# Kernel tuning notes

Measured on AMD Instinct MI355X. Metric: run time of the kernel, lower is better.

## Reference

```python
import jax, jax.numpy as jnp
import numpy as np

ALPHA = 0.2          # LeakyReLU slope
NEG_BIG = -9e15      # mask value from the torch code
LN_EPS = 1e-5        # torch LayerNorm default eps
GAT_SCALE = 1.0


def _layer_norm(x, g, b):
    mu = x.mean(-1, keepdims=True)
    var = ((x - mu) ** 2).mean(-1, keepdims=True)
    return (x - mu) * jax.lax.rsqrt(var + LN_EPS) * g + b


def _gat_layer(h, adj, W, a, concat):
    # h: [B,N,Fin], adj: [N,N] weighted, W: [Fin,Fout], a: [2*Fout,1]
    Wh = jnp.einsum('bnf,fo->bno', h, W)                 # [B,N,Fout]
    Fo = W.shape[1]
    a_i, a_j = a[:Fo, 0], a[Fo:, 0]
    # e[b,i,j] = leakyrelu(Wh[b,i].a_i + Wh[b,j].a_j)  (== cat([Wh_i,Wh_j]) @ a)
    e = jax.nn.leaky_relu(
        (Wh @ a_i)[:, :, None] + (Wh @ a_j)[:, None, :], ALPHA)  # [B,N,N]
    att = jnp.where(adj[None, :, :] > 0, e, NEG_BIG)
    att = jax.nn.softmax(att, axis=2)
    att = att * adj[None, :, :]
    att = att / (att.sum(axis=2, keepdims=True) + 1e-8)
    h_prime = jnp.einsum('bij,bjo->bio', att, Wh)        # [B,N,Fout]
    return jax.nn.elu(h_prime) if concat else h_prime


def setup_inputs() -> dict:
    B, N, H, ID = 1024, 128, 64, 8
    GIN = 1 + ID  # node_feat_dim = 0
    key = jax.random.key(0)
    ks = jax.random.split(key, 20)
    # sparse weighted adjacency with self-loops
    w = jax.random.uniform(ks[0], (N, N))
    m = (jax.random.uniform(ks[1], (N, N)) < 0.3).astype(jnp.float32)
    adj = w * m + jnp.eye(N, dtype=jnp.float32)
    sc = lambda k, s: jax.random.normal(k, s, jnp.float32) * 0.1
    return {
        'c_values': jax.random.normal(ks[2], (B, N), jnp.float32),
        'adj': adj,
        'agent_emb': sc(ks[3], (N, ID)),
        'W1': sc(ks[4], (GIN, H)), 'a1': sc(ks[5], (2 * H, 1)),
        'W2': sc(ks[6], (H, H)),   'a2': sc(ks[7], (2 * H, 1)),
        'ln1_g': jnp.ones((H,)), 'ln1_b': jnp.zeros((H,)),
        'ln2_g': jnp.ones((H,)), 'ln2_b': jnp.zeros((H,)),
        'head_gat_w': sc(ks[8], (H, 1)), 'head_gat_b': jnp.zeros((1,)),
        'mlp1_w': sc(ks[9], (N, H)),  'mlp1_b': jnp.zeros((H,)),
        'mlp2_w': sc(ks[10], (H, H)), 'mlp2_b': jnp.zeros((H,)),
        'head_mlp_w': sc(ks[11], (H, 1)), 'head_mlp_b': jnp.zeros((1,)),
        'gate1_w': sc(ks[12], (N, H)), 'gate1_b': jnp.zeros((H,)),
        'gate2_w': sc(ks[13], (H, 1)), 'gate2_b': jnp.full((1,), -5.0),
    }


def reference(c_values, adj, agent_emb, W1, a1, W2, a2,
              ln1_g, ln1_b, ln2_g, ln2_b, head_gat_w, head_gat_b,
              mlp1_w, mlp1_b, mlp2_w, mlp2_b, head_mlp_w, head_mlp_b,
              gate1_w, gate1_b, gate2_w, gate2_b):
    B, N = c_values.shape
    # node features: [c_value, agent_id_embedding]
    id_feat = jnp.broadcast_to(agent_emb[None], (B, N, agent_emb.shape[1]))
    x_g = jnp.concatenate([c_values[..., None], id_feat], axis=-1)  # [B,N,9]
    h1 = _gat_layer(x_g, adj, W1, a1, concat=True)
    h1 = _layer_norm(h1, ln1_g, ln1_b)
    h2 = _gat_layer(h1, adj, W2, a2, concat=False)
    h = jax.nn.relu(h2 + h1)
    h = _layer_norm(h, ln2_g, ln2_b)
    q_gat = h.mean(axis=1) @ head_gat_w + head_gat_b                # [B,1]
    x_m = jax.nn.relu(c_values @ mlp1_w + mlp1_b)
    x_m = jax.nn.relu(x_m @ mlp2_w + mlp2_b)
    q_mlp = x_m @ head_mlp_w + head_mlp_b                           # [B,1]
    gate = jax.nn.sigmoid(
        jax.nn.relu(c_values @ gate1_w + gate1_b) @ gate2_w + gate2_b)
    return q_mlp + gate * GAT_SCALE * q_gat
```

## Files before the change

kernel.cpp:

```cpp
#include <hip/hip_runtime.h>

typedef unsigned short u16;
typedef unsigned int u32;
typedef short v8s __attribute__((ext_vector_type(8)));
typedef float v4f __attribute__((ext_vector_type(4)));
typedef float v2f __attribute__((ext_vector_type(2)));

__device__ __forceinline__ float bflo(u32 d){union{u32 i;float f;}u;u.i=d<<16;return u.f;}
__device__ __forceinline__ float bfhi(u32 d){union{u32 i;float f;}u;u.i=d&0xffff0000u;return u.f;}
__device__ __forceinline__ u16 f2bfr(float f){union{float f;u32 i;}u;u.f=f;return (u16)((u.i+0x8000u)>>16);}
__device__ __forceinline__ u32 pk2bf(float a,float b){
    union{float f;u32 i;}ua,ub; ua.f=a; ub.f=b;
    u32 x = ua.i + 0x8000u, y = ub.i + 0x8000u;
    return __builtin_amdgcn_perm(y, x, 0x07060302);
}
__device__ __forceinline__ v8s pack8(const float* w){
    union { uint4 u; v8s v; } c;
    c.u.x = pk2bf(w[0],w[1]); c.u.y = pk2bf(w[2],w[3]);
    c.u.z = pk2bf(w[4],w[5]); c.u.w = pk2bf(w[6],w[7]);
    return c.v;
}

__device__ __forceinline__ void flash_att(
    int wv, int l15, int q4,
    const float* __restrict__ ADJ,
    const float* __restrict__ sEi, const float* __restrict__ sFi,
    const float* __restrict__ sEj, const float* __restrict__ sFj,
    const u16* __restrict__ sWhT,
    v4f acc[2][4], float invD[2])
{
    const int r0 = 16*wv + l15, r1 = r0 + 64;
    const v2f Ei0 = {sEi[r0], sEi[r0]}, Fi0 = {sFi[r0], sFi[r0]};
    const v2f Ei1 = {sEi[r1], sEi[r1]}, Fi1 = {sFi[r1], sFi[r1]};
    v2f D0 = {0.f,0.f}, D1 = {0.f,0.f};
    #pragma unroll
    for (int s = 0; s < 2; ++s)
        #pragma unroll
        for (int ct = 0; ct < 4; ++ct) acc[s][ct] = (v4f){0.f,0.f,0.f,0.f};

    #pragma unroll
    for (int ks = 0; ks < 4; ++ks) {
        const int ko = ks*32 + q4*8;
        const v2f* Ejp = (const v2f*)(sEj + ko);
        const v2f* Fjp = (const v2f*)(sFj + ko);
        const v2f* A0p = (const v2f*)(ADJ + r0*128 + ko);
        const v2f* A1p = (const v2f*)(ADJ + r1*128 + ko);
        union { u32 u[4]; v8s v; } P0, P1;
        #pragma unroll
        for (int p = 0; p < 4; ++p) {
            v2f E = Ejp[p], F = Fjp[p];
            v2f a0 = A0p[p], a1 = A1p[p];
            v2f m0 = __builtin_elementwise_max(Ei0*E, Fi0*F);
            v2f m1 = __builtin_elementwise_max(Ei1*E, Fi1*F);
            v2f x0 = m0 * a0;
            v2f x1 = m1 * a1;
            D0 += x0; D1 += x1;
            P0.u[p] = pk2bf(x0.x, x0.y);
            P1.u[p] = pk2bf(x1.x, x1.y);
        }
        #pragma unroll
        for (int ct = 0; ct < 4; ++ct) {
            v8s B = *(const v8s*)(sWhT + (16*ct + l15)*136 + ko);
            acc[0][ct] = __builtin_amdgcn_mfma_f32_16x16x32_bf16(P0.v, B, acc[0][ct], 0,0,0);
            acc[1][ct] = __builtin_amdgcn_mfma_f32_16x16x32_bf16(P1.v, B, acc[1][ct], 0,0,0);
        }
    }
    float d0 = D0.x + D0.y, d1 = D1.x + D1.y;
    d0 += __shfl_xor(d0, 16); d0 += __shfl_xor(d0, 32);
    d1 += __shfl_xor(d1, 16); d1 += __shfl_xor(d1, 32);
    invD[0] = 1.f / d0; invD[1] = 1.f / d1;
}

__global__ __launch_bounds__(256, 5) void graphmixer_kernel(
    const float* __restrict__ C,
    const float* __restrict__ ADJ,
    const float* __restrict__ EMB,
    const float* __restrict__ W1,
    const float* __restrict__ A1,
    const float* __restrict__ W2,
    const float* __restrict__ A2,
    const float* __restrict__ LN1G, const float* __restrict__ LN1B,
    const float* __restrict__ LN2G, const float* __restrict__ LN2B,
    const float* __restrict__ HGW,  const float* __restrict__ HGB,
    const float* __restrict__ MLP1W, const float* __restrict__ MLP1B,
    const float* __restrict__ MLP2W, const float* __restrict__ MLP2B,
    const float* __restrict__ HMW,  const float* __restrict__ HMB,
    const float* __restrict__ G1W,  const float* __restrict__ G1B,
    const float* __restrict__ G2W,  const float* __restrict__ G2B,
    float* __restrict__ OUT)
{
    const int b = blockIdx.x, t = threadIdx.x;
    const int lane = t & 63, wv = t >> 6;
    const int l15 = lane & 15, q4 = lane >> 4;

    __shared__ __align__(16) unsigned char smem[26272];
    u16*   R1   = (u16*)(smem);
    float* sEi  = (float*)(smem + 18432);
    float* sFi  = (float*)(smem + 18944);
    float* sEj  = (float*)(smem + 19456);
    float* sFj  = (float*)(smem + 19968);
    float* sScr = (float*)(smem + 20480);
    float* v2i  = (float*)(smem + 21024);
    float* v2j  = (float*)(smem + 21280);
    float* v1i  = (float*)(smem + 21536);
    float* v1j  = (float*)(smem + 21600);
    float* sEmb = (float*)(smem + 21664);
    float* sC   = (float*)(smem + 25760);
    float* colp = (float*)(smem + 21664);

    const float* Cb = C + b*128;

    if (wv == 0) {
        #pragma unroll
        for (int q = 0; q < 4; ++q)
            ((float4*)sEmb)[lane + 64*q] = ((const float4*)EMB)[lane + 64*q];
        if (lane < 32) ((float4*)sC)[lane] = ((const float4*)Cb)[lane];
        if (lane >= 32 && lane < 41) {
            int f = lane - 32; float a = 0.f;
            for (int q = 0; q < 16; ++q) {
                float4 w = *(const float4*)(W1 + f*64 + q*4);
                float4 x = *(const float4*)(A1 + q*4);
                a += w.x*x.x + w.y*x.y + w.z*x.z + w.w*x.w;
            }
            v1i[f] = a;
        } else if (lane >= 48 && lane < 57) {
            int f = lane - 48; float a = 0.f;
            for (int q = 0; q < 16; ++q) {
                float4 w = *(const float4*)(W1 + f*64 + q*4);
                float4 x = *(const float4*)(A1 + 64 + q*4);
                a += w.x*x.x + w.y*x.y + w.z*x.z + w.w*x.w;
            }
            v1j[f] = a;
        }
    } else if (wv == 3) {
        float ai = 0.f, aj = 0.f;
        for (int q = 0; q < 16; ++q) {
            float4 w  = *(const float4*)(W2 + lane*64 + q*4);
            float4 xi = *(const float4*)(A2 + q*4);
            float4 xj = *(const float4*)(A2 + 64 + q*4);
            ai += w.x*xi.x + w.y*xi.y + w.z*xi.z + w.w*xi.w;
            aj += w.x*xj.x + w.y*xj.y + w.z*xj.z + w.w*xj.w;
        }
        v2i[lane] = ai; v2j[lane] = aj;
    } else if (wv == 1) {
        float a = 0.f;
        for (int k = 0; k < 128; k += 4) {
            float4 c4 = *(const float4*)(Cb + k);
            a += c4.x*MLP1W[k*64+lane] + c4.y*MLP1W[(k+1)*64+lane]
               + c4.z*MLP1W[(k+2)*64+lane] + c4.w*MLP1W[(k+3)*64+lane];
        }
        sScr[lane] = fmaxf(a + MLP1B[lane], 0.f);
        float a2 = 0.f;
        for (int k = 0; k < 64; ++k) a2 += sScr[k] * MLP2W[k*64 + lane];
        float x2 = fmaxf(a2 + MLP2B[lane], 0.f);
        float p1 = x2 * HMW[lane];
        #pragma unroll
        for (int off = 32; off >= 1; off >>= 1) p1 += __shfl_down(p1, off);
        if (lane == 0) sScr[128] = p1 + HMB[0];
    } else {
        float a = 0.f;
        for (int k = 0; k < 128; k += 4) {
            float4 c4 = *(const float4*)(Cb + k);
            a += c4.x*G1W[k*64+lane] + c4.y*G1W[(k+1)*64+lane]
               + c4.z*G1W[(k+2)*64+lane] + c4.w*G1W[(k+3)*64+lane];
        }
        float g1 = fmaxf(a + G1B[lane], 0.f);
        float p2 = g1 * G2W[lane];
        #pragma unroll
        for (int off = 32; off >= 1; off >>= 1) p2 += __shfl_down(p2, off);
        if (lane == 0) sScr[129] = 1.f / (1.f + __expf(-(p2 + G2B[0])));
    }
    __syncthreads();

    {
        v8s Af[2];
        #pragma unroll
        for (int s = 0; s < 2; ++s) {
            const int row = 16*(wv + 4*s) + l15;
            float av[8];
            #pragma unroll
            for (int j = 0; j < 8; ++j) av[j] = 0.f;
            if (q4 == 0) {
                av[0] = sC[row];
                float4 e0 = *(const float4*)(sEmb + row*8);
                float4 e1 = *(const float4*)(sEmb + row*8 + 4);
                av[1]=e0.x; av[2]=e0.y; av[3]=e0.z; av[4]=e0.w;
                av[5]=e1.x; av[6]=e1.y; av[7]=e1.z;
            } else if (q4 == 1) {
                av[0] = sEmb[row*8 + 7];
            }
            Af[s] = pack8(av);
        }
        #pragma unroll
        for (int ct = 0; ct < 4; ++ct) {
            const int col = 16*ct + l15;
            float bv[8];
            #pragma unroll
            for (int j = 0; j < 8; ++j) bv[j] = 0.f;
            if (q4 == 0) {
                #pragma unroll
                for (int j = 0; j < 8; ++j) bv[j] = W1[j*64 + col];
            } else if (q4 == 1) {
                bv[0] = W1[8*64 + col];
            }
            v8s Bf1 = pack8(bv);
            v4f a0 = (v4f){0.f,0.f,0.f,0.f}, a1 = (v4f){0.f,0.f,0.f,0.f};
            a0 = __builtin_amdgcn_mfma_f32_16x16x32_bf16(Af[0], Bf1, a0, 0,0,0);
            a1 = __builtin_amdgcn_mfma_f32_16x16x32_bf16(Af[1], Bf1, a1, 0,0,0);
            uint2 p0, p1;
            p0.x = pk2bf(a0[0], a0[1]); p0.y = pk2bf(a0[2], a0[3]);
            p1.x = pk2bf(a1[0], a1[1]); p1.y = pk2bf(a1[2], a1[3]);
            *(uint2*)(R1 + col*136 + 16*wv      + 4*q4) = p0;
            *(uint2*)(R1 + col*136 + 16*(wv+4)  + 4*q4) = p1;
        }
    }
    {
        const int row = t >> 1;
        const float* vv = (t & 1) ? v1j : v1i;
        float c = sC[row];
        float4 e0 = *(const float4*)(sEmb + row*8);
        float4 e1 = *(const float4*)(sEmb + row*8 + 4);
        float e = c*vv[0] + e0.x*vv[1]+e0.y*vv[2]+e0.z*vv[3]+e0.w*vv[4]
                          + e1.x*vv[5]+e1.y*vv[6]+e1.z*vv[7]+e1.w*vv[8];
        if (t & 1) { sEj[row] = __expf(e); sFj[row] = __expf(0.2f*e); }
        else       { sEi[row] = __expf(e); sFi[row] = __expf(0.2f*e); }
    }
    __syncthreads();

    uint2 h1p[2][4];
    {
        v4f acc[2][4]; float invD[2];
        flash_att(wv, l15, q4, ADJ, sEi, sFi, sEj, sFj, R1, acc, invD);
        __syncthreads();

        float g4[4], b4[4], v2i4[4], v2j4[4];
        #pragma unroll
        for (int ct = 0; ct < 4; ++ct) {
            g4[ct] = LN1G[16*ct + l15]; b4[ct] = LN1B[16*ct + l15];
            v2i4[ct] = v2i[16*ct + l15]; v2j4[ct] = v2j[16*ct + l15];
        }
        #pragma unroll
        for (int s = 0; s < 2; ++s) {
            float hprev[4];
            #pragma unroll
            for (int reg = 0; reg < 4; ++reg) {
                const int ro = 16*(wv + 4*s) + 4*q4 + reg;
                const float rd = __shfl(invD[s], 4*q4 + reg);
                float x[4], s1 = 0.f, s2 = 0.f;
                #pragma unroll
                for (int ct = 0; ct < 4; ++ct) {
                    float v = acc[s][ct][reg] * rd;
                    v = (v > 0.f) ? v : (__expf(v) - 1.f);
                    x[ct] = v; s1 += v; s2 += v*v;
                }
                s1 += __shfl_xor(s1, 1); s2 += __shfl_xor(s2, 1);
                s1 += __shfl_xor(s1, 2); s2 += __shfl_xor(s2, 2);
                s1 += __shfl_xor(s1, 4); s2 += __shfl_xor(s2, 4);
                s1 += __shfl_xor(s1, 8); s2 += __shfl_xor(s2, 8);
                const float mean = s1 * (1.f/64.f);
                const float var  = s2 * (1.f/64.f) - mean*mean;
                const float rstd = rsqrtf(var + 1e-5f);
                float pi = 0.f, pj = 0.f;
                #pragma unroll
                for (int ct = 0; ct < 4; ++ct) {
                    float h = (x[ct] - mean) * rstd * g4[ct] + b4[ct];
                    R1[ro*72 + 16*ct + l15] = f2bfr(h);
                    pi += h * v2i4[ct]; pj += h * v2j4[ct];
                    if ((reg & 1) == 0) hprev[ct] = h;
                    else if (reg == 1)  h1p[s][ct].x = pk2bf(hprev[ct], h);
                    else                h1p[s][ct].y = pk2bf(hprev[ct], h);
                }
                pi += __shfl_xor(pi, 1); pj += __shfl_xor(pj, 1);
                pi += __shfl_xor(pi, 2); pj += __shfl_xor(pj, 2);
                pi += __shfl_xor(pi, 4); pj += __shfl_xor(pj, 4);
                pi += __shfl_xor(pi, 8); pj += __shfl_xor(pj, 8);
                if (l15 == 0) {
                    sEi[ro] = __expf(pi); sFi[ro] = __expf(0.2f*pi);
                    sEj[ro] = __expf(pj); sFj[ro] = __expf(0.2f*pj);
                }
            }
        }
    }
    __syncthreads();

    {
        v8s Afrag[2][2];
        #pragma unroll
        for (int s = 0; s < 2; ++s)
            #pragma unroll
            for (int ks = 0; ks < 2; ++ks)
                Afrag[s][ks] = *(const v8s*)(R1 + (16*(wv+4*s) + l15)*72 + ks*32 + q4*8);
        __syncthreads();

        v4f acc2[2][4];
        #pragma unroll
        for (int s = 0; s < 2; ++s)
            #pragma unroll
            for (int ct = 0; ct < 4; ++ct) acc2[s][ct] = (v4f){0.f,0.f,0.f,0.f};
        #pragma unroll
        for (int ks = 0; ks < 2; ++ks) {
            const int kb = ks*32 + q4*8;
            #pragma unroll
            for (int ct = 0; ct < 4; ++ct) {
                const float* wp = W2 + kb*64 + 16*ct + l15;
                float w8[8];
                #pragma unroll
                for (int j = 0; j < 8; ++j) w8[j] = wp[j*64];
                v8s Bf = pack8(w8);
                #pragma unroll
                for (int s = 0; s < 2; ++s)
                    acc2[s][ct] = __builtin_amdgcn_mfma_f32_16x16x32_bf16(Afrag[s][ks], Bf, acc2[s][ct], 0,0,0);
            }
        }
        #pragma unroll
        for (int s = 0; s < 2; ++s) {
            const int rb = 16*(wv+4*s) + 4*q4;
            #pragma unroll
            for (int ct = 0; ct < 4; ++ct) {
                const int col = 16*ct + l15;
                uint2 p;
                p.x = pk2bf(acc2[s][ct][0], acc2[s][ct][1]);
                p.y = pk2bf(acc2[s][ct][2], acc2[s][ct][3]);
                *(uint2*)(R1 + col*136 + rb) = p;
            }
        }
    }
    __syncthreads();

    {
        v4f acc[2][4]; float invD[2];
        flash_att(wv, l15, q4, ADJ, sEi, sFi, sEj, sFj, R1, acc, invD);

        float g4[4], b4[4], colsum[4];
        #pragma unroll
        for (int ct = 0; ct < 4; ++ct) {
            g4[ct] = LN2G[16*ct + l15]; b4[ct] = LN2B[16*ct + l15]; colsum[ct] = 0.f;
        }
        #pragma unroll
        for (int s = 0; s < 2; ++s) {
            #pragma unroll
            for (int reg = 0; reg < 4; ++reg) {
                const float rd = __shfl(invD[s], 4*q4 + reg);
                float x[4], s1 = 0.f, s2 = 0.f;
                #pragma unroll
                for (int ct = 0; ct < 4; ++ct) {
                    u32 w = (reg < 2) ? h1p[s][ct].x : h1p[s][ct].y;
                    float h1v = (reg & 1) ? bfhi(w) : bflo(w);
                    float v = fmaxf(acc[s][ct][reg] * rd + h1v, 0.f);
                    x[ct] = v; s1 += v; s2 += v*v;
                }
                s1 += __shfl_xor(s1, 1); s2 += __shfl_xor(s2, 1);
                s1 += __shfl_xor(s1, 2); s2 += __shfl_xor(s2, 2);
                s1 += __shfl_xor(s1, 4); s2 += __shfl_xor(s2, 4);
                s1 += __shfl_xor(s1, 8); s2 += __shfl_xor(s2, 8);
                const float mean = s1 * (1.f/64.f);
                const float var  = s2 * (1.f/64.f) - mean*mean;
                const float rstd = rsqrtf(var + 1e-5f);
                #pragma unroll
                for (int ct = 0; ct < 4; ++ct)
                    colsum[ct] += (x[ct] - mean) * rstd * g4[ct] + b4[ct];
            }
        }
        #pragma unroll
        for (int ct = 0; ct < 4; ++ct) {
            colsum[ct] += __shfl_xor(colsum[ct], 16);
            colsum[ct] += __shfl_xor(colsum[ct], 32);
        }
        if (lane < 16) {
            #pragma unroll
            for (int ct = 0; ct < 4; ++ct) colp[wv*64 + ct*16 + lane] = colsum[ct];
        }
    }
    __syncthreads();

    if (wv == 0) {
        float s = colp[lane] + colp[64 + lane] + colp[128 + lane] + colp[192 + lane];
        float p = s * (1.f/128.f) * HGW[lane];
        #pragma unroll
        for (int off = 32; off >= 1; off >>= 1) p += __shfl_down(p, off);
        if (lane == 0) OUT[b] = sScr[128] + sScr[129] * (p + HGB[0]);
    }
}

extern "C" void kernel_launch(void* const* d_in, const int* in_sizes, int n_in,
                              void* d_out, int out_size, void* d_ws, size_t ws_size,
                              hipStream_t stream) {
    (void)n_in; (void)out_size; (void)d_ws; (void)ws_size;
    const float* C     = (const float*)d_in[0];
    const float* ADJ   = (const float*)d_in[1];
    const float* EMB   = (const float*)d_in[2];
    const float* W1    = (const float*)d_in[3];
    const float* A1    = (const float*)d_in[4];
    const float* W2    = (const float*)d_in[5];
    const float* A2    = (const float*)d_in[6];
    const float* LN1G  = (const float*)d_in[7];
    const float* LN1B  = (const float*)d_in[8];
    const float* LN2G  = (const float*)d_in[9];
    const float* LN2B  = (const float*)d_in[10];
    const float* HGW   = (const float*)d_in[11];
    const float* HGB   = (const float*)d_in[12];
    const float* MLP1W = (const float*)d_in[13];
    const float* MLP1B = (const float*)d_in[14];
    const float* MLP2W = (const float*)d_in[15];
    const float* MLP2B = (const float*)d_in[16];
    const float* HMW   = (const float*)d_in[17];
    const float* HMB   = (const float*)d_in[18];
    const float* G1W   = (const float*)d_in[19];
    const float* G1B   = (const float*)d_in[20];
    const float* G2W   = (const float*)d_in[21];
    const float* G2B   = (const float*)d_in[22];

    const int B = in_sizes[0] / 128;

    graphmixer_kernel<<<dim3(B), dim3(256), 0, stream>>>(
        C, ADJ, EMB, W1, A1, W2, A2, LN1G, LN1B, LN2G, LN2B,
        HGW, HGB, MLP1W, MLP1B, MLP2W, MLP2B, HMW, HMB,
        G1W, G1B, G2W, G2B, (float*)d_out);
}
```

Baseline: 135.4 us.

## Process two batch elements per block to share adjacency loads and weights

Each block now handles two batch samples instead of one, so the grid is halved. Adjacency values read from global memory in the attention loop, the W2 B-fragments, and embedding/setup work are shared across both samples, and the extra independent MFMA chains give more instruction-level parallelism. In exchange, shared memory per block nearly doubles, register pressure rises (launch bounds drop from 5 to 2 blocks per CU), and only 512 blocks remain, which may underfill the GPU and reduce latency hiding.

Result: no change. 133.7 us (-1.2%).

```diff
diff --git a/kernel.cpp b/kernel.cpp
--- a/kernel.cpp
+++ b/kernel.cpp
@@ -21,57 +21,182 @@
     return c.v;
 }
 
-__device__ __forceinline__ void flash_att(
-    int wv, int l15, int q4,
-    const float* __restrict__ ADJ,
-    const float* __restrict__ sEi, const float* __restrict__ sFi,
-    const float* __restrict__ sEj, const float* __restrict__ sFj,
-    const u16* __restrict__ sWhT,
-    v4f acc[2][4], float invD[2])
+__device__ __forceinline__ void flash_att2(
+    int wv, int l15, int q4, const float* __restrict__ ADJ,
+    const float* __restrict__ sEiA, const float* __restrict__ sFiA,
+    const float* __restrict__ sEjA, const float* __restrict__ sFjA,
+    const float* __restrict__ sEiB, const float* __restrict__ sFiB,
+    const float* __restrict__ sEjB, const float* __restrict__ sFjB,
+    const u16* __restrict__ R1A, const u16* __restrict__ R1B,
+    v4f accA[2][4], v4f accB[2][4], float invDA[2], float invDB[2])
 {
     const int r0 = 16*wv + l15, r1 = r0 + 64;
-    const v2f Ei0 = {sEi[r0], sEi[r0]}, Fi0 = {sFi[r0], sFi[r0]};
-    const v2f Ei1 = {sEi[r1], sEi[r1]}, Fi1 = {sFi[r1], sFi[r1]};
-    v2f D0 = {0.f,0.f}, D1 = {0.f,0.f};
+    const v2f EiA0={sEiA[r0],sEiA[r0]}, FiA0={sFiA[r0],sFiA[r0]};
+    const v2f EiA1={sEiA[r1],sEiA[r1]}, FiA1={sFiA[r1],sFiA[r1]};
+    const v2f EiB0={sEiB[r0],sEiB[r0]}, FiB0={sFiB[r0],sFiB[r0]};
+    const v2f EiB1={sEiB[r1],sEiB[r1]}, FiB1={sFiB[r1],sFiB[r1]};
+    v2f DA0={0.f,0.f}, DA1={0.f,0.f}, DB0={0.f,0.f}, DB1={0.f,0.f};
     #pragma unroll
     for (int s = 0; s < 2; ++s)
         #pragma unroll
-        for (int ct = 0; ct < 4; ++ct) acc[s][ct] = (v4f){0.f,0.f,0.f,0.f};
+        for (int ct = 0; ct < 4; ++ct) {
+            accA[s][ct] = (v4f){0.f,0.f,0.f,0.f};
+            accB[s][ct] = (v4f){0.f,0.f,0.f,0.f};
+        }
 
     #pragma unroll
     for (int ks = 0; ks < 4; ++ks) {
         const int ko = ks*32 + q4*8;
-        const v2f* Ejp = (const v2f*)(sEj + ko);
-        const v2f* Fjp = (const v2f*)(sFj + ko);
+        const v2f* EjA = (const v2f*)(sEjA + ko);
+        const v2f* FjA = (const v2f*)(sFjA + ko);
+        const v2f* EjB = (const v2f*)(sEjB + ko);
+        const v2f* FjB = (const v2f*)(sFjB + ko);
         const v2f* A0p = (const v2f*)(ADJ + r0*128 + ko);
         const v2f* A1p = (const v2f*)(ADJ + r1*128 + ko);
-        union { u32 u[4]; v8s v; } P0, P1;
+        union { u32 u[4]; v8s v; } PA0, PA1, PB0, PB1;
         #pragma unroll
         for (int p = 0; p < 4; ++p) {
-            v2f E = Ejp[p], F = Fjp[p];
             v2f a0 = A0p[p], a1 = A1p[p];
-            v2f m0 = __builtin_elementwise_max(Ei0*E, Fi0*F);
-            v2f m1 = __builtin_elementwise_max(Ei1*E, Fi1*F);
-            v2f x0 = m0 * a0;
-            v2f x1 = m1 * a1;
-            D0 += x0; D1 += x1;
-            P0.u[p] = pk2bf(x0.x, x0.y);
-            P1.u[p] = pk2bf(x1.x, x1.y);
+            v2f EA = EjA[p], FA = FjA[p];
+            v2f EB = EjB[p], FB = FjB[p];
+            v2f xA0 = __builtin_elementwise_max(EiA0*EA, FiA0*FA) * a0;
+            v2f xA1 = __builtin_elementwise_max(EiA1*EA, FiA1*FA) * a1;
+            v2f xB0 = __builtin_elementwise_max(EiB0*EB, FiB0*FB) * a0;
+            v2f xB1 = __builtin_elementwise_max(EiB1*EB, FiB1*FB) * a1;
+            DA0 += xA0; DA1 += xA1; DB0 += xB0; DB1 += xB1;
+            PA0.u[p] = pk2bf(xA0.x, xA0.y);
+            PA1.u[p] = pk2bf(xA1.x, xA1.y);
+            PB0.u[p] = pk2bf(xB0.x, xB0.y);
+            PB1.u[p] = pk2bf(xB1.x, xB1.y);
         }
         #pragma unroll
         for (int ct = 0; ct < 4; ++ct) {
-            v8s B = *(const v8s*)(sWhT + (16*ct + l15)*136 + ko);
-            acc[0][ct] = __builtin_amdgcn_mfma_f32_16x16x32_bf16(P0.v, B, acc[0][ct], 0,0,0);
-            acc[1][ct] = __builtin_amdgcn_mfma_f32_16x16x32_bf16(P1.v, B, acc[1][ct], 0,0,0);
-        }
-    }
-    float d0 = D0.x + D0.y, d1 = D1.x + D1.y;
-    d0 += __shfl_xor(d0, 16); d0 += __shfl_xor(d0, 32);
-    d1 += __shfl_xor(d1, 16); d1 += __shfl_xor(d1, 32);
-    invD[0] = 1.f / d0; invD[1] = 1.f / d1;
-}
-
-__global__ __launch_bounds__(256, 5) void graphmixer_kernel(
+            v8s BA = *(const v8s*)(R1A + (16*ct + l15)*136 + ko);
+            v8s BB = *(const v8s*)(R1B + (16*ct + l15)*136 + ko);
+            accA[0][ct] = __builtin_amdgcn_mfma_f32_16x16x32_bf16(PA0.v, BA, accA[0][ct], 0,0,0);
+            accA[1][ct] = __builtin_amdgcn_mfma_f32_16x16x32_bf16(PA1.v, BA, accA[1][ct], 0,0,0);
+            accB[0][ct] = __builtin_amdgcn_mfma_f32_16x16x32_bf16(PB0.v, BB, accB[0][ct], 0,0,0);
+            accB[1][ct] = __builtin_amdgcn_mfma_f32_16x16x32_bf16(PB1.v, BB, accB[1][ct], 0,0,0);
+        }
+    }
+    float dA0 = DA0.x + DA0.y, dA1 = DA1.x + DA1.y;
+    float dB0 = DB0.x + DB0.y, dB1 = DB1.x + DB1.y;
+    dA0 += __shfl_xor(dA0, 16); dA0 += __shfl_xor(dA0, 32);
+    dA1 += __shfl_xor(dA1, 16); dA1 += __shfl_xor(dA1, 32);
+    dB0 += __shfl_xor(dB0, 16); dB0 += __shfl_xor(dB0, 32);
+    dB1 += __shfl_xor(dB1, 16); dB1 += __shfl_xor(dB1, 32);
+    invDA[0] = 1.f / dA0; invDA[1] = 1.f / dA1;
+    invDB[0] = 1.f / dB0; invDB[1] = 1.f / dB1;
+}
+
+__device__ __forceinline__ void epi1(
+    int wv, int l15, int q4,
+    const v4f acc[2][4], const float invD[2],
+    const float* __restrict__ LN1G, const float* __restrict__ LN1B,
+    const float* __restrict__ v2i, const float* __restrict__ v2j,
+    u16* __restrict__ R1,
+    float* __restrict__ sEi, float* __restrict__ sFi,
+    float* __restrict__ sEj, float* __restrict__ sFj,
+    uint2 h1p[2][4])
+{
+    float g4[4], b4[4], v2i4[4], v2j4[4];
+    #pragma unroll
+    for (int ct = 0; ct < 4; ++ct) {
+        g4[ct] = LN1G[16*ct + l15]; b4[ct] = LN1B[16*ct + l15];
+        v2i4[ct] = v2i[16*ct + l15]; v2j4[ct] = v2j[16*ct + l15];
+    }
+    #pragma unroll
+    for (int s = 0; s < 2; ++s) {
+        float hprev[4];
+        #pragma unroll
+        for (int reg = 0; reg < 4; ++reg) {
+            const int ro = 16*(wv + 4*s) + 4*q4 + reg;
+            const float rd = __shfl(invD[s], 4*q4 + reg);
+            float x[4], s1 = 0.f, s2 = 0.f;
+            #pragma unroll
+            for (int ct = 0; ct < 4; ++ct) {
+                float v = acc[s][ct][reg] * rd;
+                v = (v > 0.f) ? v : (__expf(v) - 1.f);
+                x[ct] = v; s1 += v; s2 += v*v;
+            }
+            s1 += __shfl_xor(s1, 1); s2 += __shfl_xor(s2, 1);
+            s1 += __shfl_xor(s1, 2); s2 += __shfl_xor(s2, 2);
+            s1 += __shfl_xor(s1, 4); s2 += __shfl_xor(s2, 4);
+            s1 += __shfl_xor(s1, 8); s2 += __shfl_xor(s2, 8);
+            const float mean = s1 * (1.f/64.f);
+            const float var  = s2 * (1.f/64.f) - mean*mean;
+            const float rstd = rsqrtf(var + 1e-5f);
+            float pi = 0.f, pj = 0.f;
+            #pragma unroll
+            for (int ct = 0; ct < 4; ++ct) {
+                float h = (x[ct] - mean) * rstd * g4[ct] + b4[ct];
+                R1[ro*72 + 16*ct + l15] = f2bfr(h);
+                pi += h * v2i4[ct]; pj += h * v2j4[ct];
+                if ((reg & 1) == 0) hprev[ct] = h;
+                else if (reg == 1)  h1p[s][ct].x = pk2bf(hprev[ct], h);
+                else                h1p[s][ct].y = pk2bf(hprev[ct], h);
+            }
+            pi += __shfl_xor(pi, 1); pj += __shfl_xor(pj, 1);
+            pi += __shfl_xor(pi, 2); pj += __shfl_xor(pj, 2);
+            pi += __shfl_xor(pi, 4); pj += __shfl_xor(pj, 4);
+            pi += __shfl_xor(pi, 8); pj += __shfl_xor(pj, 8);
+            if (l15 == 0) {
+                sEi[ro] = __expf(pi); sFi[ro] = __expf(0.2f*pi);
+                sEj[ro] = __expf(pj); sFj[ro] = __expf(0.2f*pj);
+            }
+        }
+    }
+}
+
+__device__ __forceinline__ void epi2(
+    int lane, int wv, int l15, int q4,
+    const v4f acc[2][4], const float invD[2],
+    const uint2 h1p[2][4],
+    const float* __restrict__ LN2G, const float* __restrict__ LN2B,
+    float* __restrict__ colp)
+{
+    float g4[4], b4[4], colsum[4];
+    #pragma unroll
+    for (int ct = 0; ct < 4; ++ct) {
+        g4[ct] = LN2G[16*ct + l15]; b4[ct] = LN2B[16*ct + l15]; colsum[ct] = 0.f;
+    }
+    #pragma unroll
+    for (int s = 0; s < 2; ++s) {
+        #pragma unroll
+        for (int reg = 0; reg < 4; ++reg) {
+            const float rd = __shfl(invD[s], 4*q4 + reg);
+            float x[4], s1 = 0.f, s2 = 0.f;
+            #pragma unroll
+            for (int ct = 0; ct < 4; ++ct) {
+                u32 w = (reg < 2) ? h1p[s][ct].x : h1p[s][ct].y;
+                float h1v = (reg & 1) ? bfhi(w) : bflo(w);
+                float v = fmaxf(acc[s][ct][reg] * rd + h1v, 0.f);
+                x[ct] = v; s1 += v; s2 += v*v;
+            }
+            s1 += __shfl_xor(s1, 1); s2 += __shfl_xor(s2, 1);
+            s1 += __shfl_xor(s1, 2); s2 += __shfl_xor(s2, 2);
+            s1 += __shfl_xor(s1, 4); s2 += __shfl_xor(s2, 4);
+            s1 += __shfl_xor(s1, 8); s2 += __shfl_xor(s2, 8);
+            const float mean = s1 * (1.f/64.f);
+            const float var  = s2 * (1.f/64.f) - mean*mean;
+            const float rstd = rsqrtf(var + 1e-5f);
+            #pragma unroll
+            for (int ct = 0; ct < 4; ++ct)
+                colsum[ct] += (x[ct] - mean) * rstd * g4[ct] + b4[ct];
+        }
+    }
+    #pragma unroll
+    for (int ct = 0; ct < 4; ++ct) {
+        colsum[ct] += __shfl_xor(colsum[ct], 16);
+        colsum[ct] += __shfl_xor(colsum[ct], 32);
+    }
+    if (lane < 16) {
+        #pragma unroll
+        for (int ct = 0; ct < 4; ++ct) colp[wv*64 + ct*16 + lane] = colsum[ct];
+    }
+}
+
+__global__ __launch_bounds__(256, 2) void graphmixer_kernel(
     const float* __restrict__ C,
     const float* __restrict__ ADJ,
     const float* __restrict__ EMB,
@@ -89,32 +214,43 @@
     const float* __restrict__ G2W,  const float* __restrict__ G2B,
     float* __restrict__ OUT)
 {
-    const int b = blockIdx.x, t = threadIdx.x;
+    const int bx = blockIdx.x, t = threadIdx.x;
     const int lane = t & 63, wv = t >> 6;
     const int l15 = lane & 15, q4 = lane >> 4;
-
-    __shared__ __align__(16) unsigned char smem[26272];
-    u16*   R1   = (u16*)(smem);
-    float* sEi  = (float*)(smem + 18432);
-    float* sFi  = (float*)(smem + 18944);
-    float* sEj  = (float*)(smem + 19456);
-    float* sFj  = (float*)(smem + 19968);
-    float* sScr = (float*)(smem + 20480);
-    float* v2i  = (float*)(smem + 21024);
-    float* v2j  = (float*)(smem + 21280);
-    float* v1i  = (float*)(smem + 21536);
-    float* v1j  = (float*)(smem + 21600);
-    float* sEmb = (float*)(smem + 21664);
-    float* sC   = (float*)(smem + 25760);
-    float* colp = (float*)(smem + 21664);
-
-    const float* Cb = C + b*128;
+    const int bA = 2*bx, bB = 2*bx + 1;
+
+    __shared__ __align__(16) unsigned char smem[47808];
+    u16*   R1A  = (u16*)(smem);
+    u16*   R1B  = (u16*)(smem + 18432);
+    float* sEiA = (float*)(smem + 36864);
+    float* sFiA = (float*)(smem + 37376);
+    float* sEjA = (float*)(smem + 37888);
+    float* sFjA = (float*)(smem + 38400);
+    float* sEiB = (float*)(smem + 38912);
+    float* sFiB = (float*)(smem + 39424);
+    float* sEjB = (float*)(smem + 39936);
+    float* sFjB = (float*)(smem + 40448);
+    float* v2i  = (float*)(smem + 40960);
+    float* v2j  = (float*)(smem + 41216);
+    float* v1i  = (float*)(smem + 41472);
+    float* v1j  = (float*)(smem + 41536);
+    float* sScrA= (float*)(smem + 41600);
+    float* sScrB= (float*)(smem + 42144);
+    float* sEmb = (float*)(smem + 42688);
+    float* sCA  = (float*)(smem + 46784);
+    float* sCB  = (float*)(smem + 47296);
+    float* colpA= (float*)(smem + 42688);
+    float* colpB= (float*)(smem + 43712);
+
+    const float* CbA = C + bA*128;
+    const float* CbB = C + bB*128;
 
     if (wv == 0) {
         #pragma unroll
         for (int q = 0; q < 4; ++q)
             ((float4*)sEmb)[lane + 64*q] = ((const float4*)EMB)[lane + 64*q];
-        if (lane < 32) ((float4*)sC)[lane] = ((const float4*)Cb)[lane];
+        if (lane < 32) ((float4*)sCA)[lane] = ((const float4*)CbA)[lane];
+        else           ((float4*)sCB)[lane - 32] = ((const float4*)CbB)[lane - 32];
         if (lane >= 32 && lane < 41) {
             int f = lane - 32; float a = 0.f;
             for (int q = 0; q < 16; ++q) {
@@ -132,7 +268,48 @@
             }
             v1j[f] = a;
         }
-    } else if (wv == 3) {
+        float a = 0.f;
+        for (int k = 0; k < 128; k += 4) {
+            float4 c4 = *(const float4*)(CbB + k);
+            a += c4.x*G1W[k*64+lane] + c4.y*G1W[(k+1)*64+lane]
+               + c4.z*G1W[(k+2)*64+lane] + c4.w*G1W[(k+3)*64+lane];
+        }
+        float g1 = fmaxf(a + G1B[lane], 0.f);
+        float p2 = g1 * G2W[lane];
+        #pragma unroll
+        for (int off = 32; off >= 1; off >>= 1) p2 += __shfl_down(p2, off);
+        if (lane == 0) sScrB[129] = 1.f / (1.f + __expf(-(p2 + G2B[0])));
+    } else if (wv == 1) {
+        float a = 0.f;
+        for (int k = 0; k < 128; k += 4) {
+            float4 c4 = *(const float4*)(CbA + k);
+            a += c4.x*MLP1W[k*64+lane] + c4.y*MLP1W[(k+1)*64+lane]
+               + c4.z*MLP1W[(k+2)*64+lane] + c4.w*MLP1W[(k+3)*64+lane];
+        }
+        sScrA[lane] = fmaxf(a + MLP1B[lane], 0.f);
+        float a2 = 0.f;
+        for (int k = 0; k < 64; ++k) a2 += sScrA[k] * MLP2W[k*64 + lane];
+        float x2 = fmaxf(a2 + MLP2B[lane], 0.f);
+        float p1 = x2 * HMW[lane];
+        #pragma unroll
+        for (int off = 32; off >= 1; off >>= 1) p1 += __shfl_down(p1, off);
+        if (lane == 0) sScrA[128] = p1 + HMB[0];
+    } else if (wv == 2) {
+        float a = 0.f;
+        for (int k = 0; k < 128; k += 4) {
+            float4 c4 = *(const float4*)(CbB + k);
+            a += c4.x*MLP1W[k*64+lane] + c4.y*MLP1W[(k+1)*64+lane]
+               + c4.z*MLP1W[(k+2)*64+lane] + c4.w*MLP1W[(k+3)*64+lane];
+        }
+        sScrB[lane] = fmaxf(a + MLP1B[lane], 0.f);
+        float a2 = 0.f;
+        for (int k = 0; k < 64; ++k) a2 += sScrB[k] * MLP2W[k*64 + lane];
+        float x2 = fmaxf(a2 + MLP2B[lane], 0.f);
+        float p1 = x2 * HMW[lane];
+        #pragma unroll
+        for (int off = 32; off >= 1; off >>= 1) p1 += __shfl_down(p1, off);
+        if (lane == 0) sScrB[128] = p1 + HMB[0];
+    } else {
         float ai = 0.f, aj = 0.f;
         for (int q = 0; q < 16; ++q) {
             float4 w  = *(const float4*)(W2 + lane*64 + q*4);
@@ -142,25 +319,9 @@
             aj += w.x*xj.x + w.y*xj.y + w.z*xj.z + w.w*xj.w;
         }
         v2i[lane] = ai; v2j[lane] = aj;
-    } else if (wv == 1) {
         float a = 0.f;
         for (int k = 0; k < 128; k += 4) {
-            float4 c4 = *(const float4*)(Cb + k);
-            a += c4.x*MLP1W[k*64+lane] + c4.y*MLP1W[(k+1)*64+lane]
-               + c4.z*MLP1W[(k+2)*64+lane] + c4.w*MLP1W[(k+3)*64+lane];
-        }
-        sScr[lane] = fmaxf(a + MLP1B[lane], 0.f);
-        float a2 = 0.f;
-        for (int k = 0; k < 64; ++k) a2 += sScr[k] * MLP2W[k*64 + lane];
-        float x2 = fmaxf(a2 + MLP2B[lane], 0.f);
-        float p1 = x2 * HMW[lane];
-        #pragma unroll
-        for (int off = 32; off >= 1; off >>= 1) p1 += __shfl_down(p1, off);
-        if (lane == 0) sScr[128] = p1 + HMB[0];
-    } else {
-        float a = 0.f;
-        for (int k = 0; k < 128; k += 4) {
-            float4 c4 = *(const float4*)(Cb + k);
+            float4 c4 = *(const float4*)(CbA + k);
             a += c4.x*G1W[k*64+lane] + c4.y*G1W[(k+1)*64+lane]
                + c4.z*G1W[(k+2)*64+lane] + c4.w*G1W[(k+3)*64+lane];
         }
@@ -168,28 +329,32 @@
         float p2 = g1 * G2W[lane];
         #pragma unroll
         for (int off = 32; off >= 1; off >>= 1) p2 += __shfl_down(p2, off);
-        if (lane == 0) sScr[129] = 1.f / (1.f + __expf(-(p2 + G2B[0])));
+        if (lane == 0) sScrA[129] = 1.f / (1.f + __expf(-(p2 + G2B[0])));
     }
     __syncthreads();
 
     {
-        v8s Af[2];
+        v8s AfA[2], AfB[2];
         #pragma unroll
         for (int s = 0; s < 2; ++s) {
             const int row = 16*(wv + 4*s) + l15;
-            float av[8];
-            #pragma unroll
-            for (int j = 0; j < 8; ++j) av[j] = 0.f;
+            float avA[8], avB[8];
+            #pragma unroll
+            for (int j = 0; j < 8; ++j) { avA[j] = 0.f; avB[j] = 0.f; }
             if (q4 == 0) {
-                av[0] = sC[row];
                 float4 e0 = *(const float4*)(sEmb + row*8);
                 float4 e1 = *(const float4*)(sEmb + row*8 + 4);
-                av[1]=e0.x; av[2]=e0.y; av[3]=e0.z; av[4]=e0.w;
-                av[5]=e1.x; av[6]=e1.y; av[7]=e1.z;
+                avA[0] = sCA[row];
+                avA[1]=e0.x; avA[2]=e0.y; avA[3]=e0.z; avA[4]=e0.w;
+                avA[5]=e1.x; avA[6]=e1.y; avA[7]=e1.z;
+                avB[0] = sCB[row];
+                avB[1]=e0.x; avB[2]=e0.y; avB[3]=e0.z; avB[4]=e0.w;
+                avB[5]=e1.x; avB[6]=e1.y; avB[7]=e1.z;
             } else if (q4 == 1) {
-                av[0] = sEmb[row*8 + 7];
-            }
-            Af[s] = pack8(av);
+                avA[0] = sEmb[row*8 + 7];
+                avB[0] = sEmb[row*8 + 7];
+            }
+            AfA[s] = pack8(avA); AfB[s] = pack8(avB);
         }
         #pragma unroll
         for (int ct = 0; ct < 4; ++ct) {
@@ -204,99 +369,76 @@
                 bv[0] = W1[8*64 + col];
             }
             v8s Bf1 = pack8(bv);
-            v4f a0 = (v4f){0.f,0.f,0.f,0.f}, a1 = (v4f){0.f,0.f,0.f,0.f};
-            a0 = __builtin_amdgcn_mfma_f32_16x16x32_bf16(Af[0], Bf1, a0, 0,0,0);
-            a1 = __builtin_amdgcn_mfma_f32_16x16x32_bf16(Af[1], Bf1, a1, 0,0,0);
-            uint2 p0, p1;
-            p0.x = pk2bf(a0[0], a0[1]); p0.y = pk2bf(a0[2], a0[3]);
-            p1.x = pk2bf(a1[0], a1[1]); p1.y = pk2bf(a1[2], a1[3]);
-            *(uint2*)(R1 + col*136 + 16*wv      + 4*q4) = p0;
-            *(uint2*)(R1 + col*136 + 16*(wv+4)  + 4*q4) = p1;
+            v4f aA0 = (v4f){0.f,0.f,0.f,0.f}, aA1 = (v4f){0.f,0.f,0.f,0.f};
+            v4f aB0 = (v4f){0.f,0.f,0.f,0.f}, aB1 = (v4f){0.f,0.f,0.f,0.f};
+            aA0 = __builtin_amdgcn_mfma_f32_16x16x32_bf16(AfA[0], Bf1, aA0, 0,0,0);
+            aA1 = __builtin_amdgcn_mfma_f32_16x16x32_bf16(AfA[1], Bf1, aA1, 0,0,0);
+            aB0 = __builtin_amdgcn_mfma_f32_16x16x32_bf16(AfB[0], Bf1, aB0, 0,0,0);
+            aB1 = __builtin_amdgcn_mfma_f32_16x16x32_bf16(AfB[1], Bf1, aB1, 0,0,0);
+            uint2 p;
+            p.x = pk2bf(aA0[0], aA0[1]); p.y = pk2bf(aA0[2], aA0[3]);
+            *(uint2*)(R1A + col*136 + 16*wv     + 4*q4) = p;
+            p.x = pk2bf(aA1[0], aA1[1]); p.y = pk2bf(aA1[2], aA1[3]);
+            *(uint2*)(R1A + col*136 + 16*(wv+4) + 4*q4) = p;
+            p.x = pk2bf(aB0[0], aB0[1]); p.y = pk2bf(aB0[2], aB0[3]);
+            *(uint2*)(R1B + col*136 + 16*wv     + 4*q4) = p;
+            p.x = pk2bf(aB1[0], aB1[1]); p.y = pk2bf(aB1[2], aB1[3]);
+            *(uint2*)(R1B + col*136 + 16*(wv+4) + 4*q4) = p;
         }
     }
     {
         const int row = t >> 1;
         const float* vv = (t & 1) ? v1j : v1i;
-        float c = sC[row];
         float4 e0 = *(const float4*)(sEmb + row*8);
         float4 e1 = *(const float4*)(sEmb + row*8 + 4);
-        float e = c*vv[0] + e0.x*vv[1]+e0.y*vv[2]+e0.z*vv[3]+e0.w*vv[4]
-                          + e1.x*vv[5]+e1.y*vv[6]+e1.z*vv[7]+e1.w*vv[8];
-        if (t & 1) { sEj[row] = __expf(e); sFj[row] = __expf(0.2f*e); }
-        else       { sEi[row] = __expf(e); sFi[row] = __expf(0.2f*e); }
+        float base = e0.x*vv[1]+e0.y*vv[2]+e0.z*vv[3]+e0.w*vv[4]
+                   + e1.x*vv[5]+e1.y*vv[6]+e1.z*vv[7]+e1.w*vv[8];
+        float eA = sCA[row]*vv[0] + base;
+        float eB = sCB[row]*vv[0] + base;
+        if (t & 1) {
+            sEjA[row] = __expf(eA); sFjA[row] = __expf(0.2f*eA);
+            sEjB[row] = __expf(eB); sFjB[row] = __expf(0.2f*eB);
+        } else {
+            sEiA[row] = __expf(eA); sFiA[row] = __expf(0.2f*eA);
+            sEiB[row] = __expf(eB); sFiB[row] = __expf(0.2f*eB);
+        }
     }
     __syncthreads();
 
-    uint2 h1p[2][4];
+    uint2 h1pA[2][4], h1pB[2][4];
     {
-        v4f acc[2][4]; float invD[2];
-        flash_att(wv, l15, q4, ADJ, sEi, sFi, sEj, sFj, R1, acc, invD);
+        v4f accA[2][4], accB[2][4]; float invDA[2], invDB[2];
+        flash_att2(wv, l15, q4, ADJ,
+                   sEiA, sFiA, sEjA, sFjA, sEiB, sFiB, sEjB, sFjB,
+                   R1A, R1B, accA, accB, invDA, invDB);
         __syncthreads();
 
-        float g4[4], b4[4], v2i4[4], v2j4[4];
-        #pragma unroll
-        for (int ct = 0; ct < 4; ++ct) {
-            g4[ct] = LN1G[16*ct + l15]; b4[ct] = LN1B[16*ct + l15];
-            v2i4[ct] = v2i[16*ct + l15]; v2j4[ct] = v2j[16*ct + l15];
-        }
-        #pragma unroll
-        for (int s = 0; s < 2; ++s) {
-            float hprev[4];
-            #pragma unroll
-            for (int reg = 0; reg < 4; ++reg) {
-                const int ro = 16*(wv + 4*s) + 4*q4 + reg;
-                const float rd = __shfl(invD[s], 4*q4 + reg);
-                float x[4], s1 = 0.f, s2 = 0.f;
-                #pragma unroll
-                for (int ct = 0; ct < 4; ++ct) {
-                    float v = acc[s][ct][reg] * rd;
-                    v = (v > 0.f) ? v : (__expf(v) - 1.f);
-                    x[ct] = v; s1 += v; s2 += v*v;
-                }
-                s1 += __shfl_xor(s1, 1); s2 += __shfl_xor(s2, 1);
-                s1 += __shfl_xor(s1, 2); s2 += __shfl_xor(s2, 2);
-                s1 += __shfl_xor(s1, 4); s2 += __shfl_xor(s2, 4);
-                s1 += __shfl_xor(s1, 8); s2 += __shfl_xor(s2, 8);
-                const float mean = s1 * (1.f/64.f);
-                const float var  = s2 * (1.f/64.f) - mean*mean;
-                const float rstd = rsqrtf(var + 1e-5f);
-                float pi = 0.f, pj = 0.f;
-                #pragma unroll
-                for (int ct = 0; ct < 4; ++ct) {
-                    float h = (x[ct] - mean) * rstd * g4[ct] + b4[ct];
-                    R1[ro*72 + 16*ct + l15] = f2bfr(h);
-                    pi += h * v2i4[ct]; pj += h * v2j4[ct];
-                    if ((reg & 1) == 0) hprev[ct] = h;
-                    else if (reg == 1)  h1p[s][ct].x = pk2bf(hprev[ct], h);
-                    else                h1p[s][ct].y = pk2bf(hprev[ct], h);
-                }
-                pi += __shfl_xor(pi, 1); pj += __shfl_xor(pj, 1);
-                pi += __shfl_xor(pi, 2); pj += __shfl_xor(pj, 2);
-                pi += __shfl_xor(pi, 4); pj += __shfl_xor(pj, 4);
-                pi += __shfl_xor(pi, 8); pj += __shfl_xor(pj, 8);
-                if (l15 == 0) {
-                    sEi[ro] = __expf(pi); sFi[ro] = __expf(0.2f*pi);
-                    sEj[ro] = __expf(pj); sFj[ro] = __expf(0.2f*pj);
-                }
-            }
-        }
+        epi1(wv, l15, q4, accA, invDA, LN1G, LN1B, v2i, v2j,
+             R1A, sEiA, sFiA, sEjA, sFjA, h1pA);
+        epi1(wv, l15, q4, accB, invDB, LN1G, LN1B, v2i, v2j,
+             R1B, sEiB, sFiB, sEjB, sFjB, h1pB);
     }
     __syncthreads();
 
     {
-        v8s Afrag[2][2];
+        v8s AfrA[2][2], AfrB[2][2];
         #pragma unroll
         for (int s = 0; s < 2; ++s)
             #pragma unroll
-            for (int ks = 0; ks < 2; ++ks)
-                Afrag[s][ks] = *(const v8s*)(R1 + (16*(wv+4*s) + l15)*72 + ks*32 + q4*8);
+            for (int ks = 0; ks < 2; ++ks) {
+                AfrA[s][ks] = *(const v8s*)(R1A + (16*(wv+4*s) + l15)*72 + ks*32 + q4*8);
+                AfrB[s][ks] = *(const v8s*)(R1B + (16*(wv+4*s) + l15)*72 + ks*32 + q4*8);
+            }
         __syncthreads();
 
-        v4f acc2[2][4];
+        v4f acA[2][4], acB[2][4];
         #pragma unroll
         for (int s = 0; s < 2; ++s)
             #pragma unroll
-            for (int ct = 0; ct < 4; ++ct) acc2[s][ct] = (v4f){0.f,0.f,0.f,0.f};
+            for (int ct = 0; ct < 4; ++ct) {
+                acA[s][ct] = (v4f){0.f,0.f,0.f,0.f};
+                acB[s][ct] = (v4f){0.f,0.f,0.f,0.f};
+            }
         #pragma unroll
         for (int ks = 0; ks < 2; ++ks) {
             const int kb = ks*32 + q4*8;
@@ -308,8 +450,10 @@
                 for (int j = 0; j < 8; ++j) w8[j] = wp[j*64];
                 v8s Bf = pack8(w8);
                 #pragma unroll
-                for (int s = 0; s < 2; ++s)
-                    acc2[s][ct] = __builtin_amdgcn_mfma_f32_16x16x32_bf16(Afrag[s][ks], Bf, acc2[s][ct], 0,0,0);
+                for (int s = 0; s < 2; ++s) {
+                    acA[s][ct] = __builtin_amdgcn_mfma_f32_16x16x32_bf16(AfrA[s][ks], Bf, acA[s][ct], 0,0,0);
+                    acB[s][ct] = __builtin_amdgcn_mfma_f32_16x16x32_bf16(AfrB[s][ks], Bf, acB[s][ct], 0,0,0);
+                }
             }
         }
         #pragma unroll
@@ -319,66 +463,39 @@
             for (int ct = 0; ct < 4; ++ct) {
                 const int col = 16*ct + l15;
                 uint2 p;
-                p.x = pk2bf(acc2[s][ct][0], acc2[s][ct][1]);
-                p.y = pk2bf(acc2[s][ct][2], acc2[s][ct][3]);
-                *(uint2*)(R1 + col*136 + rb) = p;
+                p.x = pk2bf(acA[s][ct][0], acA[s][ct][1]);
+                p.y = pk2bf(acA[s][ct][2], acA[s][ct][3]);
+                *(uint2*)(R1A + col*136 + rb) = p;
+                p.x = pk2bf(acB[s][ct][0], acB[s][ct][1]);
+                p.y = pk2bf(acB[s][ct][2], acB[s][ct][3]);
+                *(uint2*)(R1B + col*136 + rb) = p;
             }
         }
     }
     __syncthreads();
 
     {
-        v4f acc[2][4]; float invD[2];
-        flash_att(wv, l15, q4, ADJ, sEi, sFi, sEj, sFj, R1, acc, invD);
-
-        float g4[4], b4[4], colsum[4];
-        #pragma unroll
-        for (int ct = 0; ct < 4; ++ct) {
-            g4[ct] = LN2G[16*ct + l15]; b4[ct] = LN2B[16*ct + l15]; colsum[ct] = 0.f;
-        }
-        #pragma unroll
-        for (int s = 0; s < 2; ++s) {
-            #pragma unroll
-            for (int reg = 0; reg < 4; ++reg) {
-                const float rd = __shfl(invD[s], 4*q4 + reg);
-                float x[4], s1 = 0.f, s2 = 0.f;
-                #pragma unroll
-                for (int ct = 0; ct < 4; ++ct) {
-                    u32 w = (reg < 2) ? h1p[s][ct].x : h1p[s][ct].y;
-                    float h1v = (reg & 1) ? bfhi(w) : bflo(w);
-                    float v = fmaxf(acc[s][ct][reg] * rd + h1v, 0.f);
-                    x[ct] = v; s1 += v; s2 += v*v;
-                }
-                s1 += __shfl_xor(s1, 1); s2 += __shfl_xor(s2, 1);
-                s1 += __shfl_xor(s1, 2); s2 += __shfl_xor(s2, 2);
-                s1 += __shfl_xor(s1, 4); s2 += __shfl_xor(s2, 4);
-                s1 += __shfl_xor(s1, 8); s2 += __shfl_xor(s2, 8);
-                const float mean = s1 * (1.f/64.f);
-                const float var  = s2 * (1.f/64.f) - mean*mean;
-                const float rstd = rsqrtf(var + 1e-5f);
-                #pragma unroll
-                for (int ct = 0; ct < 4; ++ct)
-                    colsum[ct] += (x[ct] - mean) * rstd * g4[ct] + b4[ct];
-            }
-        }
-        #pragma unroll
-        for (int ct = 0; ct < 4; ++ct) {
-            colsum[ct] += __shfl_xor(colsum[ct], 16);
-            colsum[ct] += __shfl_xor(colsum[ct], 32);
-        }
-        if (lane < 16) {
-            #pragma unroll
-            for (int ct = 0; ct < 4; ++ct) colp[wv*64 + ct*16 + lane] = colsum[ct];
-        }
+        v4f accA[2][4], accB[2][4]; float invDA[2], invDB[2];
+        flash_att2(wv, l15, q4, ADJ,
+                   sEiA, sFiA, sEjA, sFjA, sEiB, sFiB, sEjB, sFjB,
+                   R1A, R1B, accA, accB, invDA, invDB);
+        epi2(lane, wv, l15, q4, accA, invDA, h1pA, LN2G, LN2B, colpA);
+        epi2(lane, wv, l15, q4, accB, invDB, h1pB, LN2G, LN2B, colpB);
     }
     __syncthreads();
 
     if (wv == 0) {
-        float s = colp[lane] + colp[64 + lane] + colp[128 + lane] + colp[192 + lane];
+        float s = colpA[lane] + colpA[64 + lane] + colpA[128 + lane] + colpA[192 + lane];
         float p = s * (1.f/128.f) * HGW[lane];
         #pragma unroll
         for (int off = 32; off >= 1; off >>= 1) p += __shfl_down(p, off);
-        if (lane == 0) OUT[b] = sScr[128] + sScr[129] * (p + HGB[0]);
+        if (lane == 0) OUT[bA] = sScrA[128] + sScrA[129] * (p + HGB[0]);
+    } else if (wv == 1) {
+        float s = colpB[lane] + colpB[64 + lane] + colpB[128 + lane] + colpB[192 + lane];
+        float p = s * (1.f/128.f) * HGW[lane];
+        #pragma unroll
+        for (int off = 32; off >= 1; off >>= 1) p += __shfl_down(p, off);
+        if (lane == 0) OUT[bB] = sScrB[128] + sScrB[129] * (p + HGB[0]);
     }
 }
 
@@ -412,7 +529,7 @@
 
     const int B = in_sizes[0] / 128;
 
-    graphmixer_kernel<<<dim3(B), dim3(256), 0, stream>>>(
+    graphmixer_kernel<<<dim3(B/2), dim3(256), 0, stream>>>(
         C, ADJ, EMB, W1, A1, W2, A2, LN1G, LN1B, LN2G, LN2B,
         HGW, HGB, MLP1W, MLP1B, MLP2W, MLP2B, HMW, HMB,
         G1W, G1B, G2W, G2B, (float*)d_out);
```
